# Optimization experiments

Measured on AMD Instinct MI355X. Metric: run time of the kernel, lower is better.

Reference implementation:

```python
import jax, jax.numpy as jnp
import numpy as np

QMIN, QMAX = -128, 127  # int8 range

def setup_inputs() -> dict:
    key = jax.random.key(0)
    k1, k2, k3 = jax.random.split(key, 3)
    B, S, DIN, DOUT = 8, 2048, 4096, 4096
    x = jax.random.normal(k1, (B, S, DIN), dtype=jnp.float32)
    weight = jax.random.normal(k2, (DOUT, DIN), dtype=jnp.float32) * 0.02
    bias = jax.random.normal(k3, (DOUT,), dtype=jnp.float32) * 0.01
    # per-tensor asymmetric activation qparams (as produced by a calibrated observer)
    act_scale = jnp.float32(0.05)
    act_zero_point = jnp.int32(3)
    # per-output-channel symmetric weight scales (block_size = (1, in_features))
    weight_scale = jnp.max(jnp.abs(weight), axis=1) / 127.0  # [DOUT]
    return {"x": x, "weight": weight, "bias": bias,
            "act_scale": act_scale, "act_zero_point": act_zero_point,
            "weight_scale": weight_scale}

def reference(x, weight, bias, act_scale, act_zero_point, weight_scale):
    # 1) quantize activations: per-tensor asymmetric int8
    qx = jnp.clip(jnp.round(x / act_scale) + act_zero_point, QMIN, QMAX).astype(jnp.int8)
    # 2) quantize weight: per-output-channel symmetric int8 (zero_point = 0)
    qw = jnp.clip(jnp.round(weight / weight_scale[:, None]), QMIN, QMAX).astype(jnp.int8)
    acc = jnp.einsum('bsk,nk->bsn',
                     qx.astype(jnp.int32) - act_zero_point.astype(jnp.int32),
                     qw.astype(jnp.int32))  # [B, S, DOUT] int32
    # 4) dequantize: combined scale = act_scale * weight_scale[n], then bias
    out = acc.astype(jnp.float32) * (act_scale * weight_scale) + bias
    return out
```

## Files before the change

### kernel.cpp

```cpp
#include <hip/hip_runtime.h>
#include <cstdint>

#define M_DIM 16384
#define N_DIM 4096
#define K_DIM 4096

#define BM 128
#define BN 128
#define BK 64

typedef __attribute__((ext_vector_type(4))) int int32x4;

#define GLLD16(g, l)                                              \
  __builtin_amdgcn_global_load_lds(                               \
      (const __attribute__((address_space(1))) void*)(g),         \
      (__attribute__((address_space(3))) void*)(l), 16, 0, 0)

__global__ void quant_x_kernel(const float* __restrict__ x,
                               const float* __restrict__ sp,
                               const int* __restrict__ zpp,
                               int8_t* __restrict__ qx) {
  const float s = sp[0];
  const int zp = zpp[0];
  const long long t = (long long)blockIdx.x * blockDim.x + threadIdx.x;
  const float4* x4 = (const float4*)x;
  unsigned packed[4];
#pragma unroll
  for (int i = 0; i < 4; i++) {
    float4 v = x4[t * 4 + i];
    int q0 = min(127, max(-128, (int)rintf(v.x / s) + zp));
    int q1 = min(127, max(-128, (int)rintf(v.y / s) + zp));
    int q2 = min(127, max(-128, (int)rintf(v.z / s) + zp));
    int q3 = min(127, max(-128, (int)rintf(v.w / s) + zp));
    packed[i] = (unsigned)(q0 & 255) | ((unsigned)(q1 & 255) << 8) |
                ((unsigned)(q2 & 255) << 16) | ((unsigned)(q3 & 255) << 24);
  }
  int4 outv;
  outv.x = (int)packed[0]; outv.y = (int)packed[1];
  outv.z = (int)packed[2]; outv.w = (int)packed[3];
  ((int4*)qx)[t] = outv;
}

__global__ void quant_w_kernel(const float* __restrict__ w,
                               const float* __restrict__ wscale,
                               const float* __restrict__ bias,
                               const float* __restrict__ sp,
                               const int* __restrict__ zpp,
                               int8_t* __restrict__ qw,
                               float* __restrict__ cs,
                               float* __restrict__ off) {
  const int n = blockIdx.x;
  const float ws = wscale[n];
  const float s = sp[0];
  const int zp = zpp[0];
  const float4* wr = (const float4*)(w + (size_t)n * K_DIM);
  unsigned* qr = (unsigned*)(qw + (size_t)n * K_DIM);
  int sum = 0;
#pragma unroll
  for (int it = 0; it < K_DIM / (256 * 4); it++) {
    const int idx = it * 256 + threadIdx.x;
    float4 v = wr[idx];
    int q0 = min(127, max(-128, (int)rintf(v.x / ws)));
    int q1 = min(127, max(-128, (int)rintf(v.y / ws)));
    int q2 = min(127, max(-128, (int)rintf(v.z / ws)));
    int q3 = min(127, max(-128, (int)rintf(v.w / ws)));
    sum += q0 + q1 + q2 + q3;
    qr[idx] = (unsigned)(q0 & 255) | ((unsigned)(q1 & 255) << 8) |
              ((unsigned)(q2 & 255) << 16) | ((unsigned)(q3 & 255) << 24);
  }
  __shared__ int red[4];
#pragma unroll
  for (int o = 32; o > 0; o >>= 1) sum += __shfl_down(sum, o, 64);
  if ((threadIdx.x & 63) == 0) red[threadIdx.x >> 6] = sum;
  __syncthreads();
  if (threadIdx.x == 0) {
    const int tot = red[0] + red[1] + red[2] + red[3];
    const float c = s * ws;
    cs[n] = c;
    off[n] = bias[n] - (float)(zp * tot) * c;
  }
}

__global__ __launch_bounds__(256) void gemm_i8(
    const int8_t* __restrict__ qx, const int8_t* __restrict__ qw,
    const float* __restrict__ cs, const float* __restrict__ off,
    float* __restrict__ out) {
  __shared__ __align__(16) int8_t As[BM * BK];
  __shared__ __align__(16) int8_t Bs[BN * BK];

  const int tid = threadIdx.x;
  const int lane = tid & 63;
  const int wave = tid >> 6;
  const int wm = wave >> 1;
  const int wn = wave & 1;

  const int n0 = blockIdx.x * BN;
  const int m0 = blockIdx.y * BM;

  int32x4 acc[4][4] = {};

  const int ci = wave * 2;
  const int sr0 = (ci + 0) * 16 + (lane >> 2);
  const int sr1 = (ci + 1) * 16 + (lane >> 2);
  const int sc0 = (lane & 3) ^ ((sr0 >> 1) & 3);
  const int sc1 = (lane & 3) ^ ((sr1 >> 1) & 3);

  const int8_t* gA0 = qx + (size_t)(m0 + sr0) * K_DIM + sc0 * 16;
  const int8_t* gA1 = qx + (size_t)(m0 + sr1) * K_DIM + sc1 * 16;
  const int8_t* gB0 = qw + (size_t)(n0 + sr0) * K_DIM + sc0 * 16;
  const int8_t* gB1 = qw + (size_t)(n0 + sr1) * K_DIM + sc1 * 16;

  int8_t* ldsA0 = As + (ci + 0) * 1024;
  int8_t* ldsA1 = As + (ci + 1) * 1024;
  int8_t* ldsB0 = Bs + (ci + 0) * 1024;
  int8_t* ldsB1 = Bs + (ci + 1) * 1024;

  const int fr = lane & 15;
  const int quad = lane >> 4;
  const int fch = (quad ^ ((fr >> 1) & 3)) * 16;

  int aoff[4], boff[4];
#pragma unroll
  for (int t = 0; t < 4; t++) {
    aoff[t] = (wm * 64 + t * 16 + fr) * BK + fch;
    boff[t] = (wn * 64 + t * 16 + fr) * BK + fch;
  }

  for (int kt = 0; kt < K_DIM; kt += BK) {
    __syncthreads();
    GLLD16(gA0 + kt, ldsA0);
    GLLD16(gA1 + kt, ldsA1);
    GLLD16(gB0 + kt, ldsB0);
    GLLD16(gB1 + kt, ldsB1);
    __syncthreads();

    int32x4 af[4], bf[4];
#pragma unroll
    for (int t = 0; t < 4; t++) {
      af[t] = *(const int32x4*)(As + aoff[t]);
      bf[t] = *(const int32x4*)(Bs + boff[t]);
    }
#pragma unroll
    for (int tm = 0; tm < 4; tm++)
#pragma unroll
      for (int tn = 0; tn < 4; tn++)
        acc[tm][tn] = __builtin_amdgcn_mfma_i32_16x16x64_i8(
            af[tm], bf[tn], acc[tm][tn], 0, 0, 0);
  }

#pragma unroll
  for (int tn = 0; tn < 4; tn++) {
    const int col = n0 + wn * 64 + tn * 16 + fr;
    const float c = cs[col];
    const float o = off[col];
#pragma unroll
    for (int tm = 0; tm < 4; tm++) {
      const int rowb = m0 + wm * 64 + tm * 16 + quad * 4;
#pragma unroll
      for (int r = 0; r < 4; r++) {
        out[(size_t)(rowb + r) * N_DIM + col] = (float)acc[tm][tn][r] * c + o;
      }
    }
  }
}

extern "C" void kernel_launch(void* const* d_in, const int* in_sizes, int n_in,
                              void* d_out, int out_size, void* d_ws,
                              size_t ws_size, hipStream_t stream) {
  const float* x = (const float*)d_in[0];
  const float* w = (const float*)d_in[1];
  const float* bias = (const float*)d_in[2];
  const float* act_scale = (const float*)d_in[3];
  const int* zp = (const int*)d_in[4];
  const float* wscale = (const float*)d_in[5];
  float* out = (float*)d_out;

  int8_t* qx = (int8_t*)d_ws;
  int8_t* qw = qx + (size_t)M_DIM * K_DIM;
  float* cs = (float*)(qw + (size_t)N_DIM * K_DIM);
  float* off = cs + N_DIM;

  quant_x_kernel<<<16384, 256, 0, stream>>>(x, act_scale, zp, qx);
  quant_w_kernel<<<N_DIM, 256, 0, stream>>>(w, wscale, bias, act_scale, zp,
                                            qw, cs, off);
  gemm_i8<<<dim3(N_DIM / BN, M_DIM / BM), 256, 0, stream>>>(qx, qw, cs, off,
                                                            out);
}
```

Measured before the change: 798.7 us.

## Double GEMM K-tile to 128 with new LDS swizzle; use reciprocal multiply in quant

```diff
diff --git a/kernel.cpp b/kernel.cpp
--- a/kernel.cpp
+++ b/kernel.cpp
@@ -7,7 +7,7 @@
 
 #define BM 128
 #define BN 128
-#define BK 64
+#define BK 128
 
 typedef __attribute__((ext_vector_type(4))) int int32x4;
 
@@ -20,25 +20,23 @@
                                const float* __restrict__ sp,
                                const int* __restrict__ zpp,
                                int8_t* __restrict__ qx) {
-  const float s = sp[0];
+  const float inv = 1.0f / sp[0];
   const int zp = zpp[0];
-  const long long t = (long long)blockIdx.x * blockDim.x + threadIdx.x;
+  const int tid = threadIdx.x;
+  const int base = blockIdx.x * 1024;
   const float4* x4 = (const float4*)x;
-  unsigned packed[4];
+  unsigned* q4 = (unsigned*)qx;
 #pragma unroll
   for (int i = 0; i < 4; i++) {
-    float4 v = x4[t * 4 + i];
-    int q0 = min(127, max(-128, (int)rintf(v.x / s) + zp));
-    int q1 = min(127, max(-128, (int)rintf(v.y / s) + zp));
-    int q2 = min(127, max(-128, (int)rintf(v.z / s) + zp));
-    int q3 = min(127, max(-128, (int)rintf(v.w / s) + zp));
-    packed[i] = (unsigned)(q0 & 255) | ((unsigned)(q1 & 255) << 8) |
-                ((unsigned)(q2 & 255) << 16) | ((unsigned)(q3 & 255) << 24);
+    const int idx = base + i * 256 + tid;
+    float4 v = x4[idx];
+    int q0 = min(127, max(-128, (int)rintf(v.x * inv) + zp));
+    int q1 = min(127, max(-128, (int)rintf(v.y * inv) + zp));
+    int q2 = min(127, max(-128, (int)rintf(v.z * inv) + zp));
+    int q3 = min(127, max(-128, (int)rintf(v.w * inv) + zp));
+    q4[idx] = (unsigned)(q0 & 255) | ((unsigned)(q1 & 255) << 8) |
+              ((unsigned)(q2 & 255) << 16) | ((unsigned)(q3 & 255) << 24);
   }
-  int4 outv;
-  outv.x = (int)packed[0]; outv.y = (int)packed[1];
-  outv.z = (int)packed[2]; outv.w = (int)packed[3];
-  ((int4*)qx)[t] = outv;
 }
 
 __global__ void quant_w_kernel(const float* __restrict__ w,
@@ -51,6 +49,7 @@
                                float* __restrict__ off) {
   const int n = blockIdx.x;
   const float ws = wscale[n];
+  const float invw = 1.0f / ws;
   const float s = sp[0];
   const int zp = zpp[0];
   const float4* wr = (const float4*)(w + (size_t)n * K_DIM);
@@ -60,10 +59,10 @@
   for (int it = 0; it < K_DIM / (256 * 4); it++) {
     const int idx = it * 256 + threadIdx.x;
     float4 v = wr[idx];
-    int q0 = min(127, max(-128, (int)rintf(v.x / ws)));
-    int q1 = min(127, max(-128, (int)rintf(v.y / ws)));
-    int q2 = min(127, max(-128, (int)rintf(v.z / ws)));
-    int q3 = min(127, max(-128, (int)rintf(v.w / ws)));
+    int q0 = min(127, max(-128, (int)rintf(v.x * invw)));
+    int q1 = min(127, max(-128, (int)rintf(v.y * invw)));
+    int q2 = min(127, max(-128, (int)rintf(v.z * invw)));
+    int q3 = min(127, max(-128, (int)rintf(v.w * invw)));
     sum += q0 + q1 + q2 + q3;
     qr[idx] = (unsigned)(q0 & 255) | ((unsigned)(q1 & 255) << 8) |
               ((unsigned)(q2 & 255) << 16) | ((unsigned)(q3 & 255) << 24);
@@ -99,53 +98,57 @@
 
   int32x4 acc[4][4] = {};
 
-  const int ci = wave * 2;
-  const int sr0 = (ci + 0) * 16 + (lane >> 2);
-  const int sr1 = (ci + 1) * 16 + (lane >> 2);
-  const int sc0 = (lane & 3) ^ ((sr0 >> 1) & 3);
-  const int sc1 = (lane & 3) ^ ((sr1 >> 1) & 3);
-
-  const int8_t* gA0 = qx + (size_t)(m0 + sr0) * K_DIM + sc0 * 16;
-  const int8_t* gA1 = qx + (size_t)(m0 + sr1) * K_DIM + sc1 * 16;
-  const int8_t* gB0 = qw + (size_t)(n0 + sr0) * K_DIM + sc0 * 16;
-  const int8_t* gB1 = qw + (size_t)(n0 + sr1) * K_DIM + sc1 * 16;
-
-  int8_t* ldsA0 = As + (ci + 0) * 1024;
-  int8_t* ldsA1 = As + (ci + 1) * 1024;
-  int8_t* ldsB0 = Bs + (ci + 0) * 1024;
-  int8_t* ldsB1 = Bs + (ci + 1) * 1024;
+  const int8_t* gA[4];
+  const int8_t* gB[4];
+  int lof[4];
+#pragma unroll
+  for (int g = 0; g < 4; g++) {
+    const int o = g * 4096 + wave * 1024 + lane * 16;
+    const int r = o >> 7;
+    const int c = ((o >> 4) & 7) ^ (r & 7);
+    gA[g] = qx + (size_t)(m0 + r) * K_DIM + c * 16;
+    gB[g] = qw + (size_t)(n0 + r) * K_DIM + c * 16;
+    lof[g] = g * 4096 + wave * 1024;
+  }
 
   const int fr = lane & 15;
   const int quad = lane >> 4;
-  const int fch = (quad ^ ((fr >> 1) & 3)) * 16;
-
-  int aoff[4], boff[4];
+  int aoff[2][4], boff[2][4];
 #pragma unroll
-  for (int t = 0; t < 4; t++) {
-    aoff[t] = (wm * 64 + t * 16 + fr) * BK + fch;
-    boff[t] = (wn * 64 + t * 16 + fr) * BK + fch;
+  for (int ks = 0; ks < 2; ks++) {
+#pragma unroll
+    for (int t = 0; t < 4; t++) {
+      const int ar = wm * 64 + t * 16 + fr;
+      const int br = wn * 64 + t * 16 + fr;
+      const int c = ks * 4 + quad;
+      aoff[ks][t] = ar * BK + (c ^ (ar & 7)) * 16;
+      boff[ks][t] = br * BK + (c ^ (br & 7)) * 16;
+    }
   }
 
   for (int kt = 0; kt < K_DIM; kt += BK) {
     __syncthreads();
-    GLLD16(gA0 + kt, ldsA0);
-    GLLD16(gA1 + kt, ldsA1);
-    GLLD16(gB0 + kt, ldsB0);
-    GLLD16(gB1 + kt, ldsB1);
+#pragma unroll
+    for (int g = 0; g < 4; g++) GLLD16(gA[g] + kt, As + lof[g]);
+#pragma unroll
+    for (int g = 0; g < 4; g++) GLLD16(gB[g] + kt, Bs + lof[g]);
     __syncthreads();
 
-    int32x4 af[4], bf[4];
 #pragma unroll
-    for (int t = 0; t < 4; t++) {
-      af[t] = *(const int32x4*)(As + aoff[t]);
-      bf[t] = *(const int32x4*)(Bs + boff[t]);
+    for (int ks = 0; ks < 2; ks++) {
+      int32x4 af[4], bf[4];
+#pragma unroll
+      for (int t = 0; t < 4; t++) {
+        af[t] = *(const int32x4*)(As + aoff[ks][t]);
+        bf[t] = *(const int32x4*)(Bs + boff[ks][t]);
+      }
+#pragma unroll
+      for (int tm = 0; tm < 4; tm++)
+#pragma unroll
+        for (int tn = 0; tn < 4; tn++)
+          acc[tm][tn] = __builtin_amdgcn_mfma_i32_16x16x64_i8(
+              af[tm], bf[tn], acc[tm][tn], 0, 0, 0);
     }
-#pragma unroll
-    for (int tm = 0; tm < 4; tm++)
-#pragma unroll
-      for (int tn = 0; tn < 4; tn++)
-        acc[tm][tn] = __builtin_amdgcn_mfma_i32_16x16x64_i8(
-            af[tm], bf[tn], acc[tm][tn], 0, 0, 0);
   }
 
 #pragma unroll
```

Result: no change. 811.2 us (+1.6%).
